# Performance work log

Hardware: AMD Instinct MI355X
Metric: run time of the kernel (lower is better)

The kernel has to match this reference:

```python
import jax, jax.numpy as jnp
import numpy as np

B, N, R, S, H, D, HIDDEN = 4, 1028, 4, 32, 12, 64, 32
L = (2 * S - 1) ** 2  # 3969 relative-position bins


def _build_tables():
    # CPB relative-coordinate table (signed log1p-normalized offsets)
    rng = np.arange(-(S - 1), S, dtype=np.float32)
    dY, dX = np.meshgrid(rng, rng, indexing='ij')
    rel = np.stack([dY / max(S - 1, 1), dX / max(S - 1, 1)], -1).reshape(-1, 2)
    rel_table = np.sign(rel) * np.log1p(np.abs(rel))  # [L, 2]
    # 2D relative-position index table over the SxS patch grid
    Y, X = np.meshgrid(np.arange(S), np.arange(S), indexing='ij')
    flat = np.stack([Y, X], 0).reshape(2, -1)          # [2, P]
    d = flat[:, :, None] - flat[:, None, :]            # [2, P, P]
    d = np.transpose(d, (1, 2, 0)).copy()              # [P, P, 2]
    d[:, :, 0] += S - 1
    d[:, :, 1] += S - 1
    d[:, :, 0] *= 2 * S - 1
    l_idx = d.sum(-1)                                  # [P, P] in [0, L)
    idx = np.full((N, N), -1, dtype=np.int64)          # -1 sentinel for register tokens
    idx[R:, R:] = l_idx
    return jnp.asarray(rel_table, jnp.float32), jnp.asarray(idx)


def setup_inputs() -> dict:
    key = jax.random.key(0)
    ks = jax.random.split(key, 8)
    rel_table, idx_table = _build_tables()
    return {
        'q': jax.random.normal(ks[0], (B, H, N, D), jnp.float32),
        'k': jax.random.normal(ks[1], (B, H, N, D), jnp.float32),
        'v': jax.random.normal(ks[2], (B, H, N, D), jnp.float32),
        'mu': jax.random.normal(ks[3], (B, 2 * H, N), jnp.float32),
        'rel_table': rel_table,                              # [L, 2] buffer
        'W1': jax.random.normal(ks[4], (HIDDEN, 2), jnp.float32) * 0.5,
        'b1': jax.random.normal(ks[5], (HIDDEN,), jnp.float32) * 0.1,
        'W2': jax.random.normal(ks[6], (H, HIDDEN), jnp.float32) * 0.05,
        'gamma': jax.random.normal(ks[7], (H,), jnp.float32),
        'idx_table': idx_table,                              # [N, N] int64
    }


def reference(q, k, v, mu, rel_table, W1, b1, W2, gamma, idx_table):
    # CPB MLP: Linear(2->hidden) + exact GELU + Linear(hidden->H, no bias)
    hid = jax.nn.gelu(rel_table @ W1.T + b1, approximate=False)   # [L, HIDDEN]
    bt = hid @ W2.T                                               # [L, H]
    bt_ext = jnp.concatenate([jnp.zeros((1, H), bt.dtype), bt], 0)  # [L+1, H]
    bias = bt_ext[idx_table + 1]                                  # [N, N, H]; sentinel -1 -> zero row

    # per-token gates: signed log1p transform then q-side + k-side split
    mu_t = jnp.sign(mu) * jnp.log1p(jnp.abs(mu))                  # [B, 2H, N]
    mu_q, mu_k = mu_t[:, :H], mu_t[:, H:]                         # each [B, H, N]
    g = mu_q[:, :, :, None] + mu_k[:, :, None, :]                 # [B, H, N, N]
    gam = jax.nn.sigmoid(gamma)[None, :, None, None]              # [1, H, 1, 1]

    scale = 1.0 / jnp.sqrt(jnp.asarray(D, jnp.float32))
    scores = jnp.einsum('bhqd,bhkd->bhqk', q, k) * scale
    scores = scores + gam * g * jnp.transpose(bias, (2, 0, 1))[None]  # [B, H, N, N]
    attn = jax.nn.softmax(scores, axis=-1)
    return jnp.einsum('bhqk,bhkd->bhqd', attn, v)
```

## Files before the change

kernel.cpp:

```cpp
#include <hip/hip_runtime.h>

#define B_ 4
#define H_ 12
#define N_ 1028
#define D_ 64
#define R_ 4
#define L_ 3969
#define HID_ 32
#define KBLK 64
#define NT_ 17
#define NBH_ 48
#define QBLK 128
#define NQT 9
#define NWG (NBH_*NQT)
#define TBL 3973
#define LOG2E 1.4426950408889634f
#define SCL1 (0.125f*LOG2E)

typedef __attribute__((ext_vector_type(8)))  short bf16x8;
typedef __attribute__((ext_vector_type(4)))  float f32x4;
typedef __attribute__((ext_vector_type(16))) float f32x16;
typedef __attribute__((ext_vector_type(2)))  unsigned int u32x2;
typedef __attribute__((ext_vector_type(4)))  unsigned int u32x4;
typedef __attribute__((address_space(3))) unsigned int lds_u32;
typedef const __attribute__((address_space(1))) unsigned int glb_u32;

__device__ __forceinline__ unsigned pkbf(float lo, float hi) {
  unsigned r;
  asm("v_cvt_pk_bf16_f32 %0, %1, %2" : "=v"(r) : "v"(lo), "v"(hi));
  return r;
}
__device__ __forceinline__ float exp2_fast(float x) {
  float r; asm("v_exp_f32 %0, %1" : "=v"(r) : "v"(x)); return r;
}
__device__ __forceinline__ float sgnlog1p(float x) {
  float t = log1pf(fabsf(x));
  return (x > 0.f) ? t : ((x < 0.f) ? -t : 0.f);
}

__global__ __launch_bounds__(256) void prep_kernel(
    const float* __restrict__ rel, const float* __restrict__ W1,
    const float* __restrict__ b1, const float* __restrict__ W2,
    const float* __restrict__ gammag, const float* __restrict__ kg,
    const float* __restrict__ vg, const float* __restrict__ mug,
    float* __restrict__ btgf, float* __restrict__ mut,
    unsigned short* __restrict__ kv)
{
  const int blk = blockIdx.x, tid = threadIdx.x;
  if (blk < 16) {
    if (blk == 0 && tid < 48) btgf[(tid >> 2)*TBL + (tid & 3)] = 0.f;
    int l = blk*256 + tid;
    if (l < L_) {
      float r0 = rel[2*l], r1 = rel[2*l+1];
      float hid[HID_];
#pragma unroll
      for (int j = 0; j < HID_; ++j) {
        float x = W1[2*j]*r0 + W1[2*j+1]*r1 + b1[j];
        hid[j] = 0.5f * x * (1.f + erff(x * 0.70710678118654752f));
      }
#pragma unroll
      for (int h = 0; h < H_; ++h) {
        float acc = 0.f;
#pragma unroll
        for (int j = 0; j < HID_; ++j) acc += W2[h*HID_+j]*hid[j];
        float gscl = LOG2E / (1.f + __expf(-gammag[h]));
        btgf[h*TBL + 4 + l] = gscl * acc;
      }
    }
  } else if (blk < 16 + NBH_*NT_) {
    const int idx = blk - 16;
    const int bh = idx / NT_, t = idx - bh*NT_;
    const int k0 = t * KBLK;
    const float* kb = kg + (size_t)bh*N_*D_;
    const float* vb = vg + (size_t)bh*N_*D_;
    unsigned short* Ko = kv + (size_t)idx*8192;
    unsigned short* Vo = Ko + 4096;
    const int kcb = tid >> 4, d4 = (tid & 15)*4;
#pragma unroll
    for (int i = 0; i < 4; ++i) {
      int kc = kcb + i*16;
      int kr = k0 + kc; if (kr >= N_) kr = N_-1;
      f32x4 a = *(const f32x4*)(kb + (size_t)kr*D_ + d4);
      *(u32x2*)&Ko[kc*64 + (d4 ^ ((kc & 7) << 3))] = (u32x2){pkbf(a[0],a[1]), pkbf(a[2],a[3])};
    }
    const int vd0 = (tid >> 4)*4, vkc0 = (tid & 15)*4;
    const int vkc0p = ((vkc0 >> 1) & 4) | ((vkc0 << 1) & 8) | (vkc0 & 48);
    f32x4 r[4];
#pragma unroll
    for (int i = 0; i < 4; ++i) {
      int kr = k0 + vkc0 + i; if (kr >= N_) kr = N_-1;
      r[i] = *(const f32x4*)(vb + (size_t)kr*D_ + vd0);
    }
#pragma unroll
    for (int j = 0; j < 4; ++j) {
      int d = vd0 + j;
      *(u32x2*)&Vo[d*64 + (vkc0p ^ ((d & 7) << 3))] =
          (u32x2){pkbf(r[0][j],r[1][j]), pkbf(r[2][j],r[3][j])};
    }
  } else {
    int idx = (blk - (16 + NBH_*NT_))*256 + tid;
    if (idx < NBH_*N_) {
      int bh = idx / N_, n = idx - bh*N_;
      int b = bh / H_, h = bh - b*H_;
      mut[idx] = sgnlog1p(mug[((size_t)b*2*H_ + H_ + h)*N_ + n]);
    }
  }
}

__global__ __launch_bounds__(512, 2) void attn_kernel(
    const float* __restrict__ qg, const float* __restrict__ mug,
    const float* __restrict__ btgf, const float* __restrict__ mut,
    const unsigned short* __restrict__ kv, float* __restrict__ outg)
{
  __shared__ __align__(16) unsigned short KV[2][2][8192];
  __shared__ __align__(16) float btgs[TBL];

  const int tid = threadIdx.x;
  const int w = tid >> 6, lane = tid & 63, hi = lane >> 5, c = lane & 31;
  const int wp = w >> 2;
  const int wq = w & 3;

  const int orig = blockIdx.x;
  const int wg = (orig & 7)*(NWG/8) + (orig >> 3);
  const int bh = wg / NQT;
  const int qt = wg - bh*NQT;
  const int b = bh / H_, h = bh - b*H_;
  const int q0 = qt * QBLK;

  const float* qb  = qg + (size_t)bh*N_*D_;
  const float* mt  = mut + (size_t)bh*N_;
  const unsigned short* kvb = kv + (size_t)bh*NT_*8192;

  {
    const float* bth = btgf + h*TBL;
    for (int i = tid; i < TBL; i += 512) btgs[i] = bth[i];
  }

  const int qrow = q0 + 32*wq + c;
  const int qrc = qrow < N_ ? qrow : N_-1;
  bf16x8 qf[4];
#pragma unroll
  for (int m = 0; m < 4; ++m) {
    const float* p = qb + (size_t)qrc*D_ + 16*m + 8*hi;
    f32x4 a0 = *(const f32x4*)p;
    f32x4 a1 = *(const f32x4*)(p + 4);
    u32x4 qw;
    qw[0] = pkbf(a0[0]*SCL1, a0[1]*SCL1); qw[1] = pkbf(a0[2]*SCL1, a0[3]*SCL1);
    qw[2] = pkbf(a1[0]*SCL1, a1[1]*SCL1); qw[3] = pkbf(a1[2]*SCL1, a1[3]*SCL1);
    qf[m] = __builtin_bit_cast(bf16x8, qw);
  }
  const float muq_c = (qrow < N_) ? sgnlog1p(mug[((size_t)b*2*H_ + h)*N_ + qrow]) : 0.f;
  const int qi = qrow - R_;
  const bool qok = (qi >= 0) && (qrow < N_);
  const int qy = qi >> 5, qx = qi & 31;
  const int lqc = qy*63 + qx + 1988;

  const int tbeg   = wp ? 9 : 0;
  const int tcount = wp ? 8 : 9;

  auto issue = [&](int tt, int pp) {
    const char* src = (const char*)(kvb + (size_t)tt*8192) + wq*4096;
    char* dst = (char*)&KV[wp][pp][0] + wq*4096;
#pragma unroll
    for (int j = 0; j < 4; ++j) {
      int o = j*1024;
      __builtin_amdgcn_global_load_lds((glb_u32*)(src + o + lane*16),
                                       (lds_u32*)(dst + o), 16, 0, 0);
    }
  };

  float mrun = -3.0e38f, lrun = 0.f;
  f32x16 Ot[2];
#pragma unroll
  for (int blk2 = 0; blk2 < 2; ++blk2)
#pragma unroll
    for (int r = 0; r < 16; ++r) Ot[blk2][r] = 0.f;

  issue(tbeg, 0);

  for (int i = 0; i < 9; ++i) {
    const bool act = i < tcount;
    const int t = tbeg + i;
    const int k0 = t * KBLK;
    const int p = i & 1;

    asm volatile("s_waitcnt vmcnt(0)" ::: "memory");
    __syncthreads();

    f32x4 mkv[2][4];
    if (act) {
#pragma unroll
      for (int bb = 0; bb < 2; ++bb)
#pragma unroll
        for (int r2 = 0; r2 < 4; ++r2) {
          int mb = k0 + 32*bb + 8*r2 + 4*hi;
          mb = mb > 1024 ? 1024 : mb;
          mkv[bb][r2] = *(const f32x4*)&mt[mb];
        }
    }
    __builtin_amdgcn_sched_barrier(0);
    if (i + 1 < tcount) issue(t + 1, p ^ 1);

    if (act) {
      const unsigned short* Kl = &KV[wp][p][0];
      const unsigned short* Vl = &KV[wp][p][4096];

      f32x16 sc[2];
#pragma unroll
      for (int bb = 0; bb < 2; ++bb)
#pragma unroll
        for (int r = 0; r < 16; ++r) sc[bb][r] = 0.f;
      __builtin_amdgcn_s_setprio(1);
#pragma unroll
      for (int m = 0; m < 4; ++m) {
        int sw = (c & 7) << 3;
        bf16x8 ka0 = *(const bf16x8*)&Kl[c*64      + ((16*m + 8*hi) ^ sw)];
        bf16x8 ka1 = *(const bf16x8*)&Kl[(32+c)*64 + ((16*m + 8*hi) ^ sw)];
        sc[0] = __builtin_amdgcn_mfma_f32_32x32x16_bf16(ka0, qf[m], sc[0], 0, 0, 0);
        sc[1] = __builtin_amdgcn_mfma_f32_32x32x16_bf16(ka1, qf[m], sc[1], 0, 0, 0);
      }
      __builtin_amdgcn_s_setprio(0);

      float smax = -3.0e38f;
#pragma unroll
      for (int bb = 0; bb < 2; ++bb)
#pragma unroll
        for (int r2 = 0; r2 < 4; ++r2) {
          const f32x4 mk = mkv[bb][r2];
          int ki0 = k0 + 32*bb + 8*r2 + 4*hi - R_;
          int lk = (ki0 >> 5)*63 + (ki0 & 31);
          int va = lqc - lk;
          bool okq = ((unsigned)ki0 < 1024u) && qok;
          int basep = okq ? va : 3;
          f32x4 bv;
          bv[0] = btgs[basep-3]; bv[1] = btgs[basep-2];
          bv[2] = btgs[basep-1]; bv[3] = btgs[basep];
          bool mq = (ki0 < 1024);
#pragma unroll
          for (int rr = 0; rr < 4; ++rr) {
            float val = sc[bb][4*r2+rr] + (muq_c + mk[rr]) * bv[3-rr];
            val = mq ? val : -3.0e38f;
            sc[bb][4*r2+rr] = val;
            smax = fmaxf(smax, val);
          }
        }
      smax = fmaxf(smax, __shfl_xor(smax, 32));

      if (__any(smax > mrun)) {
        float mnew = fmaxf(mrun, smax);
        float corr = exp2_fast(mrun - mnew);
        lrun *= corr;
#pragma unroll
        for (int blk2 = 0; blk2 < 2; ++blk2)
#pragma unroll
          for (int r = 0; r < 16; ++r) Ot[blk2][r] *= corr;
        mrun = mnew;
      }

      float psum = 0.f;
#pragma unroll
      for (int bb = 0; bb < 2; ++bb)
#pragma unroll
        for (int r = 0; r < 16; ++r) {
          float pv = exp2_fast(sc[bb][r] - mrun);
          sc[bb][r] = pv;
          psum += pv;
        }
      psum += __shfl_xor(psum, 32);
      lrun += psum;

      u32x4 pa[4];
#pragma unroll
      for (int mm = 0; mm < 4; ++mm) {
        int bb = mm >> 1, s = (mm & 1) * 8;
#pragma unroll
        for (int j = 0; j < 4; ++j)
          pa[mm][j] = pkbf(sc[bb][s + 2*j], sc[bb][s + 2*j + 1]);
      }

      __builtin_amdgcn_s_setprio(1);
#pragma unroll
      for (int mm = 0; mm < 4; ++mm) {
        bf16x8 pfr = __builtin_bit_cast(bf16x8, pa[mm]);
        int sw = (c & 7) << 3;
        bf16x8 va0 = *(const bf16x8*)&Vl[c*64      + ((16*mm + 8*hi) ^ sw)];
        bf16x8 va1 = *(const bf16x8*)&Vl[(32+c)*64 + ((16*mm + 8*hi) ^ sw)];
        Ot[0] = __builtin_amdgcn_mfma_f32_32x32x16_bf16(va0, pfr, Ot[0], 0, 0, 0);
        Ot[1] = __builtin_amdgcn_mfma_f32_32x32x16_bf16(va1, pfr, Ot[1], 0, 0, 0);
      }
      __builtin_amdgcn_s_setprio(0);
    }
  }

  __syncthreads();
  float* sh = (float*)&KV[0][0][0];
  const int base = (wq*64 + lane)*34;
  if (wp == 1) {
#pragma unroll
    for (int blk2 = 0; blk2 < 2; ++blk2)
#pragma unroll
      for (int r = 0; r < 16; ++r) sh[base + blk2*16 + r] = Ot[blk2][r];
    sh[base + 32] = mrun;
    sh[base + 33] = lrun;
  }
  __syncthreads();
  if (wp == 0) {
    float m1 = sh[base + 32], l1 = sh[base + 33];
    float M  = fmaxf(mrun, m1);
    float w0 = exp2_fast(mrun - M), w1 = exp2_fast(m1 - M);
    float rl = 1.f / (lrun*w0 + l1*w1);
    const int qo = q0 + 32*wq + c;
    if (qo < N_) {
      float* ob = outg + ((size_t)bh*N_ + qo)*64;
#pragma unroll
      for (int blk2 = 0; blk2 < 2; ++blk2)
#pragma unroll
        for (int r2 = 0; r2 < 4; ++r2) {
          f32x4 ov;
#pragma unroll
          for (int rr = 0; rr < 4; ++rr)
            ov[rr] = (Ot[blk2][4*r2+rr]*w0 + sh[base + blk2*16 + 4*r2 + rr]*w1) * rl;
          *(f32x4*)(ob + 8*r2 + 4*hi + 32*blk2) = ov;
        }
    }
  }
}

extern "C" void kernel_launch(void* const* d_in, const int* in_sizes, int n_in,
                              void* d_out, int out_size, void* d_ws, size_t ws_size,
                              hipStream_t stream) {
  const float* q     = (const float*)d_in[0];
  const float* k     = (const float*)d_in[1];
  const float* v     = (const float*)d_in[2];
  const float* mu    = (const float*)d_in[3];
  const float* rel   = (const float*)d_in[4];
  const float* W1    = (const float*)d_in[5];
  const float* b1    = (const float*)d_in[6];
  const float* W2    = (const float*)d_in[7];
  const float* gamma = (const float*)d_in[8];

  char* wsb = (char*)d_ws;
  float* btgf = (float*)wsb;
  float* mut  = (float*)(wsb + 190704);
  unsigned short* kvimg = (unsigned short*)(wsb + 388080);

  const int prep_blocks = 16 + NBH_*NT_ + (NBH_*N_ + 255)/256;
  prep_kernel<<<dim3(prep_blocks), dim3(256), 0, stream>>>(rel, W1, b1, W2, gamma,
                                                           k, v, mu, btgf, mut, kvimg);
  attn_kernel<<<dim3(NWG), dim3(512), 0, stream>>>(q, mu, btgf, mut, kvimg,
                                                   (float*)d_out);
}
```

Measured before the change: 69.54 us.

## Switch attention to 16x16x32 MFMA tiles with 64-query blocks and full key sweep

Restructures the attention kernel from 512-thread workgroups doing a 128-query tile with a split-K across two wave groups to 256-thread workgroups doing a 64-query tile. Each wave now owns 16 queries and walks all 17 key tiles with 16x16x32 bf16 MFMAs, which removes the final cross-wavegroup merge through LDS. The V image layout in the prep kernel is permuted to match the new fragment ordering, and the mu_k gate values are staged once into LDS instead of being read from global memory every tile. The grid doubles, so the bias table is reloaded into LDS by twice as many workgroups, and each workgroup now loads every K/V tile.

```diff
diff --git a/kernel.cpp b/kernel.cpp
--- a/kernel.cpp
+++ b/kernel.cpp
@@ -10,16 +10,16 @@
 #define KBLK 64
 #define NT_ 17
 #define NBH_ 48
-#define QBLK 128
-#define NQT 9
+#define QBLK 64
+#define NQT 17
 #define NWG (NBH_*NQT)
 #define TBL 3973
+#define MUKP 1088
 #define LOG2E 1.4426950408889634f
 #define SCL1 (0.125f*LOG2E)
 
 typedef __attribute__((ext_vector_type(8)))  short bf16x8;
 typedef __attribute__((ext_vector_type(4)))  float f32x4;
-typedef __attribute__((ext_vector_type(16))) float f32x16;
 typedef __attribute__((ext_vector_type(2)))  unsigned int u32x2;
 typedef __attribute__((ext_vector_type(4)))  unsigned int u32x4;
 typedef __attribute__((address_space(3))) unsigned int lds_u32;
@@ -84,7 +84,8 @@
       *(u32x2*)&Ko[kc*64 + (d4 ^ ((kc & 7) << 3))] = (u32x2){pkbf(a[0],a[1]), pkbf(a[2],a[3])};
     }
     const int vd0 = (tid >> 4)*4, vkc0 = (tid & 15)*4;
-    const int vkc0p = ((vkc0 >> 1) & 4) | ((vkc0 << 1) & 8) | (vkc0 & 48);
+    const int loc = vkc0 & 31;
+    const int p0 = 32*(vkc0 >> 5) + 8*((loc >> 2) & 3) + 4*(loc >> 4);
     f32x4 r[4];
 #pragma unroll
     for (int i = 0; i < 4; ++i) {
@@ -94,8 +95,8 @@
 #pragma unroll
     for (int j = 0; j < 4; ++j) {
       int d = vd0 + j;
-      *(u32x2*)&Vo[d*64 + (vkc0p ^ ((d & 7) << 3))] =
-          (u32x2){pkbf(r[0][j],r[1][j]), pkbf(r[2][j],r[3][j])};
+      int addr = d*64 + ((p0 & 56) ^ ((d & 7) << 3)) + (p0 & 7);
+      *(u32x2*)&Vo[addr] = (u32x2){pkbf(r[0][j],r[1][j]), pkbf(r[2][j],r[3][j])};
     }
   } else {
     int idx = (blk - (16 + NBH_*NT_))*256 + tid;
@@ -107,18 +108,17 @@
   }
 }
 
-__global__ __launch_bounds__(512, 2) void attn_kernel(
+__global__ __launch_bounds__(256, 4) void attn_kernel(
     const float* __restrict__ qg, const float* __restrict__ mug,
     const float* __restrict__ btgf, const float* __restrict__ mut,
     const unsigned short* __restrict__ kv, float* __restrict__ outg)
 {
-  __shared__ __align__(16) unsigned short KV[2][2][8192];
+  __shared__ __align__(16) unsigned short KV[2][8192];
   __shared__ __align__(16) float btgs[TBL];
+  __shared__ __align__(16) float muks[MUKP];
 
   const int tid = threadIdx.x;
-  const int w = tid >> 6, lane = tid & 63, hi = lane >> 5, c = lane & 31;
-  const int wp = w >> 2;
-  const int wq = w & 3;
+  const int w = tid >> 6, lane = tid & 63, g = (lane >> 4), c = lane & 15;
 
   const int orig = blockIdx.x;
   const int wg = (orig & 7)*(NWG/8) + (orig >> 3);
@@ -128,26 +128,27 @@
   const int q0 = qt * QBLK;
 
   const float* qb  = qg + (size_t)bh*N_*D_;
-  const float* mt  = mut + (size_t)bh*N_;
   const unsigned short* kvb = kv + (size_t)bh*NT_*8192;
 
   {
     const float* bth = btgf + h*TBL;
-    for (int i = tid; i < TBL; i += 512) btgs[i] = bth[i];
-  }
-
-  const int qrow = q0 + 32*wq + c;
+    for (int i = tid; i < TBL; i += 256) btgs[i] = bth[i];
+    const float* mt = mut + (size_t)bh*N_;
+    for (int i = tid; i < MUKP; i += 256) muks[i] = mt[i < N_ ? i : N_-1];
+  }
+
+  const int qrow = q0 + 16*w + c;
   const int qrc = qrow < N_ ? qrow : N_-1;
-  bf16x8 qf[4];
-#pragma unroll
-  for (int m = 0; m < 4; ++m) {
-    const float* p = qb + (size_t)qrc*D_ + 16*m + 8*hi;
+  bf16x8 qf[2];
+#pragma unroll
+  for (int ch = 0; ch < 2; ++ch) {
+    const float* p = qb + (size_t)qrc*D_ + ch*32 + 8*g;
     f32x4 a0 = *(const f32x4*)p;
     f32x4 a1 = *(const f32x4*)(p + 4);
     u32x4 qw;
     qw[0] = pkbf(a0[0]*SCL1, a0[1]*SCL1); qw[1] = pkbf(a0[2]*SCL1, a0[3]*SCL1);
     qw[2] = pkbf(a1[0]*SCL1, a1[1]*SCL1); qw[3] = pkbf(a1[2]*SCL1, a1[3]*SCL1);
-    qf[m] = __builtin_bit_cast(bf16x8, qw);
+    qf[ch] = __builtin_bit_cast(bf16x8, qw);
   }
   const float muq_c = (qrow < N_) ? sgnlog1p(mug[((size_t)b*2*H_ + h)*N_ + qrow]) : 0.f;
   const int qi = qrow - R_;
@@ -155,12 +156,9 @@
   const int qy = qi >> 5, qx = qi & 31;
   const int lqc = qy*63 + qx + 1988;
 
-  const int tbeg   = wp ? 9 : 0;
-  const int tcount = wp ? 8 : 9;
-
   auto issue = [&](int tt, int pp) {
-    const char* src = (const char*)(kvb + (size_t)tt*8192) + wq*4096;
-    char* dst = (char*)&KV[wp][pp][0] + wq*4096;
+    const char* src = (const char*)(kvb + (size_t)tt*8192) + w*4096;
+    char* dst = (char*)&KV[pp][0] + w*4096;
 #pragma unroll
     for (int j = 0; j < 4; ++j) {
       int o = j*1024;
@@ -170,158 +168,118 @@
   };
 
   float mrun = -3.0e38f, lrun = 0.f;
-  f32x16 Ot[2];
-#pragma unroll
-  for (int blk2 = 0; blk2 < 2; ++blk2)
-#pragma unroll
-    for (int r = 0; r < 16; ++r) Ot[blk2][r] = 0.f;
-
-  issue(tbeg, 0);
-
-  for (int i = 0; i < 9; ++i) {
-    const bool act = i < tcount;
-    const int t = tbeg + i;
+  f32x4 O[4];
+#pragma unroll
+  for (int dt = 0; dt < 4; ++dt) O[dt] = (f32x4){0.f,0.f,0.f,0.f};
+
+  issue(0, 0);
+
+  for (int t = 0; t < NT_; ++t) {
     const int k0 = t * KBLK;
-    const int p = i & 1;
+    const int p = t & 1;
 
     asm volatile("s_waitcnt vmcnt(0)" ::: "memory");
     __syncthreads();
-
-    f32x4 mkv[2][4];
-    if (act) {
-#pragma unroll
-      for (int bb = 0; bb < 2; ++bb)
-#pragma unroll
-        for (int r2 = 0; r2 < 4; ++r2) {
-          int mb = k0 + 32*bb + 8*r2 + 4*hi;
-          mb = mb > 1024 ? 1024 : mb;
-          mkv[bb][r2] = *(const f32x4*)&mt[mb];
-        }
-    }
-    __builtin_amdgcn_sched_barrier(0);
-    if (i + 1 < tcount) issue(t + 1, p ^ 1);
-
-    if (act) {
-      const unsigned short* Kl = &KV[wp][p][0];
-      const unsigned short* Vl = &KV[wp][p][4096];
-
-      f32x16 sc[2];
-#pragma unroll
-      for (int bb = 0; bb < 2; ++bb)
-#pragma unroll
-        for (int r = 0; r < 16; ++r) sc[bb][r] = 0.f;
-      __builtin_amdgcn_s_setprio(1);
-#pragma unroll
-      for (int m = 0; m < 4; ++m) {
-        int sw = (c & 7) << 3;
-        bf16x8 ka0 = *(const bf16x8*)&Kl[c*64      + ((16*m + 8*hi) ^ sw)];
-        bf16x8 ka1 = *(const bf16x8*)&Kl[(32+c)*64 + ((16*m + 8*hi) ^ sw)];
-        sc[0] = __builtin_amdgcn_mfma_f32_32x32x16_bf16(ka0, qf[m], sc[0], 0, 0, 0);
-        sc[1] = __builtin_amdgcn_mfma_f32_32x32x16_bf16(ka1, qf[m], sc[1], 0, 0, 0);
-      }
-      __builtin_amdgcn_s_setprio(0);
-
-      float smax = -3.0e38f;
-#pragma unroll
-      for (int bb = 0; bb < 2; ++bb)
-#pragma unroll
-        for (int r2 = 0; r2 < 4; ++r2) {
-          const f32x4 mk = mkv[bb][r2];
-          int ki0 = k0 + 32*bb + 8*r2 + 4*hi - R_;
-          int lk = (ki0 >> 5)*63 + (ki0 & 31);
-          int va = lqc - lk;
-          bool okq = ((unsigned)ki0 < 1024u) && qok;
-          int basep = okq ? va : 3;
-          f32x4 bv;
-          bv[0] = btgs[basep-3]; bv[1] = btgs[basep-2];
-          bv[2] = btgs[basep-1]; bv[3] = btgs[basep];
-          bool mq = (ki0 < 1024);
-#pragma unroll
-          for (int rr = 0; rr < 4; ++rr) {
-            float val = sc[bb][4*r2+rr] + (muq_c + mk[rr]) * bv[3-rr];
-            val = mq ? val : -3.0e38f;
-            sc[bb][4*r2+rr] = val;
-            smax = fmaxf(smax, val);
-          }
-        }
-      smax = fmaxf(smax, __shfl_xor(smax, 32));
-
-      if (__any(smax > mrun)) {
-        float mnew = fmaxf(mrun, smax);
-        float corr = exp2_fast(mrun - mnew);
-        lrun *= corr;
-#pragma unroll
-        for (int blk2 = 0; blk2 < 2; ++blk2)
-#pragma unroll
-          for (int r = 0; r < 16; ++r) Ot[blk2][r] *= corr;
-        mrun = mnew;
-      }
-
-      float psum = 0.f;
-#pragma unroll
-      for (int bb = 0; bb < 2; ++bb)
-#pragma unroll
-        for (int r = 0; r < 16; ++r) {
-          float pv = exp2_fast(sc[bb][r] - mrun);
-          sc[bb][r] = pv;
-          psum += pv;
-        }
-      psum += __shfl_xor(psum, 32);
-      lrun += psum;
-
-      u32x4 pa[4];
-#pragma unroll
-      for (int mm = 0; mm < 4; ++mm) {
-        int bb = mm >> 1, s = (mm & 1) * 8;
-#pragma unroll
-        for (int j = 0; j < 4; ++j)
-          pa[mm][j] = pkbf(sc[bb][s + 2*j], sc[bb][s + 2*j + 1]);
-      }
-
-      __builtin_amdgcn_s_setprio(1);
-#pragma unroll
-      for (int mm = 0; mm < 4; ++mm) {
-        bf16x8 pfr = __builtin_bit_cast(bf16x8, pa[mm]);
-        int sw = (c & 7) << 3;
-        bf16x8 va0 = *(const bf16x8*)&Vl[c*64      + ((16*mm + 8*hi) ^ sw)];
-        bf16x8 va1 = *(const bf16x8*)&Vl[(32+c)*64 + ((16*mm + 8*hi) ^ sw)];
-        Ot[0] = __builtin_amdgcn_mfma_f32_32x32x16_bf16(va0, pfr, Ot[0], 0, 0, 0);
-        Ot[1] = __builtin_amdgcn_mfma_f32_32x32x16_bf16(va1, pfr, Ot[1], 0, 0, 0);
-      }
-      __builtin_amdgcn_s_setprio(0);
-    }
-  }
-
-  __syncthreads();
-  float* sh = (float*)&KV[0][0][0];
-  const int base = (wq*64 + lane)*34;
-  if (wp == 1) {
-#pragma unroll
-    for (int blk2 = 0; blk2 < 2; ++blk2)
-#pragma unroll
-      for (int r = 0; r < 16; ++r) sh[base + blk2*16 + r] = Ot[blk2][r];
-    sh[base + 32] = mrun;
-    sh[base + 33] = lrun;
-  }
-  __syncthreads();
-  if (wp == 0) {
-    float m1 = sh[base + 32], l1 = sh[base + 33];
-    float M  = fmaxf(mrun, m1);
-    float w0 = exp2_fast(mrun - M), w1 = exp2_fast(m1 - M);
-    float rl = 1.f / (lrun*w0 + l1*w1);
-    const int qo = q0 + 32*wq + c;
-    if (qo < N_) {
-      float* ob = outg + ((size_t)bh*N_ + qo)*64;
-#pragma unroll
-      for (int blk2 = 0; blk2 < 2; ++blk2)
-#pragma unroll
-        for (int r2 = 0; r2 < 4; ++r2) {
-          f32x4 ov;
-#pragma unroll
-          for (int rr = 0; rr < 4; ++rr)
-            ov[rr] = (Ot[blk2][4*r2+rr]*w0 + sh[base + blk2*16 + 4*r2 + rr]*w1) * rl;
-          *(f32x4*)(ob + 8*r2 + 4*hi + 32*blk2) = ov;
-        }
+    if (t + 1 < NT_) issue(t + 1, p ^ 1);
+
+    const unsigned short* Kl = &KV[p][0];
+    const unsigned short* Vl = &KV[p][4096];
+
+    f32x4 sc[4];
+#pragma unroll
+    for (int kt = 0; kt < 4; ++kt) {
+      int row = kt*16 + c;
+      int sw = (row & 7) << 3;
+      bf16x8 ka0 = *(const bf16x8*)&Kl[row*64 + ((8*g) ^ sw)];
+      bf16x8 ka1 = *(const bf16x8*)&Kl[row*64 + ((32 + 8*g) ^ sw)];
+      f32x4 s = (f32x4){0.f,0.f,0.f,0.f};
+      s = __builtin_amdgcn_mfma_f32_16x16x32_bf16(ka0, qf[0], s, 0, 0, 0);
+      s = __builtin_amdgcn_mfma_f32_16x16x32_bf16(ka1, qf[1], s, 0, 0, 0);
+      sc[kt] = s;
+    }
+
+    float smax = -3.0e38f;
+#pragma unroll
+    for (int kt = 0; kt < 4; ++kt) {
+      const f32x4 mk = *(const f32x4*)&muks[k0 + kt*16 + 4*g];
+      int ki0 = k0 + kt*16 + 4*g - R_;
+      int lk = (ki0 >> 5)*63 + (ki0 & 31);
+      int va = lqc - lk;
+      bool okq = ((unsigned)ki0 < 1024u) && qok;
+      int basep = okq ? va : 3;
+      f32x4 bv;
+      bv[0] = btgs[basep-3]; bv[1] = btgs[basep-2];
+      bv[2] = btgs[basep-1]; bv[3] = btgs[basep];
+      bool mq = (ki0 < 1024);
+      f32x4 s = sc[kt];
+#pragma unroll
+      for (int r = 0; r < 4; ++r) {
+        float val = s[r] + (muq_c + mk[r]) * bv[3-r];
+        val = mq ? val : -3.0e38f;
+        s[r] = val;
+        smax = fmaxf(smax, val);
+      }
+      sc[kt] = s;
+    }
+    smax = fmaxf(smax, __shfl_xor(smax, 16));
+    smax = fmaxf(smax, __shfl_xor(smax, 32));
+
+    if (__any(smax > mrun)) {
+      float mnew = fmaxf(mrun, smax);
+      float corr = exp2_fast(mrun - mnew);
+      lrun *= corr;
+#pragma unroll
+      for (int dt = 0; dt < 4; ++dt)
+#pragma unroll
+        for (int r = 0; r < 4; ++r) O[dt][r] *= corr;
+      mrun = mnew;
+    }
+
+    float psum = 0.f;
+#pragma unroll
+    for (int kt = 0; kt < 4; ++kt)
+#pragma unroll
+      for (int r = 0; r < 4; ++r) {
+        float pv = exp2_fast(sc[kt][r] - mrun);
+        sc[kt][r] = pv;
+        psum += pv;
+      }
+    psum += __shfl_xor(psum, 16);
+    psum += __shfl_xor(psum, 32);
+    lrun += psum;
+
+    u32x4 pa[2];
+#pragma unroll
+    for (int kh = 0; kh < 2; ++kh) {
+      pa[kh][0] = pkbf(sc[2*kh][0],   sc[2*kh][1]);
+      pa[kh][1] = pkbf(sc[2*kh][2],   sc[2*kh][3]);
+      pa[kh][2] = pkbf(sc[2*kh+1][0], sc[2*kh+1][1]);
+      pa[kh][3] = pkbf(sc[2*kh+1][2], sc[2*kh+1][3]);
+    }
+
+#pragma unroll
+    for (int kh = 0; kh < 2; ++kh) {
+      bf16x8 pfr = __builtin_bit_cast(bf16x8, pa[kh]);
+      int sw = (c & 7) << 3;
+#pragma unroll
+      for (int dt = 0; dt < 4; ++dt) {
+        int d = dt*16 + c;
+        bf16x8 va = *(const bf16x8*)&Vl[d*64 + ((32*kh + 8*g) ^ sw)];
+        O[dt] = __builtin_amdgcn_mfma_f32_16x16x32_bf16(va, pfr, O[dt], 0, 0, 0);
+      }
+    }
+  }
+
+  float rlv = 1.f / lrun;
+  const int qo = q0 + 16*w + c;
+  if (qo < N_) {
+    float* ob = outg + ((size_t)bh*N_ + qo)*64;
+#pragma unroll
+    for (int dt = 0; dt < 4; ++dt) {
+      f32x4 ov;
+#pragma unroll
+      for (int r = 0; r < 4; ++r) ov[r] = O[dt][r] * rlv;
+      *(f32x4*)(ob + dt*16 + 4*g) = ov;
     }
   }
 }
@@ -347,6 +305,6 @@
   const int prep_blocks = 16 + NBH_*NT_ + (NBH_*N_ + 255)/256;
   prep_kernel<<<dim3(prep_blocks), dim3(256), 0, stream>>>(rel, W1, b1, W2, gamma,
                                                            k, v, mu, btgf, mut, kvimg);
-  attn_kernel<<<dim3(NWG), dim3(512), 0, stream>>>(q, mu, btgf, mut, kvimg,
+  attn_kernel<<<dim3(NWG), dim3(256), 0, stream>>>(q, mu, btgf, mut, kvimg,
                                                    (float*)d_out);
 }
```

New measurement: 72.04 us. +3.6%, slower.
